# Kernel tuning notes

Measured on AMD Instinct MI355X. Metric: run time of the kernel, lower is better.

## Reference

```python
import jax, jax.numpy as jnp
import numpy as np

N_ELEM = 4
NODES = [384, 1024, 1024, 1]
ALPHA0 = 100.0


def setup_inputs() -> dict:
    key = jax.random.key(0)
    ks = jax.random.split(key, 12)
    B_ref, B_tr, A, D = 32, 64, 128, NODES[0]
    x_ref = jax.random.normal(ks[0], (B_ref, A, D), jnp.float32)
    x_train = jax.random.normal(ks[1], (B_tr, A, D), jnp.float32)
    y_ref = jax.random.normal(ks[2], (B_ref * A,), jnp.float32)
    l_ref = jax.random.randint(ks[3], (B_ref, A), 1, N_ELEM + 1).astype(jnp.int32)
    l_train = jax.random.randint(ks[4], (B_tr, A), 1, N_ELEM + 1).astype(jnp.int32)

    def lin_w(k, fi, fo):
        lim = 1.0 / np.sqrt(fi)
        return jax.random.uniform(k, (N_ELEM, fi, fo), jnp.float32, -lim, lim)

    W1 = lin_w(ks[5], NODES[0], NODES[1])
    b1 = jnp.zeros((N_ELEM, NODES[1]), jnp.float32)
    W2 = lin_w(ks[6], NODES[1], NODES[2])
    b2 = jnp.zeros((N_ELEM, NODES[2]), jnp.float32)
    W3 = lin_w(ks[7], NODES[2], NODES[3])
    b3 = jnp.zeros((N_ELEM, NODES[3]), jnp.float32)
    alpha = jnp.full((N_ELEM,), ALPHA0, jnp.float32)  # one learned alpha per subnet
    return dict(x_ref=x_ref, y_ref=y_ref, l_ref=l_ref, x_train=x_train,
                l_train=l_train, W1=W1, b1=b1, W2=W2, b2=b2, W3=W3, b3=b3,
                alpha=alpha)


def reference(x_ref, y_ref, l_ref, x_train, l_train, W1, b1, W2, b2, W3, b3, alpha):
    D = x_train.shape[-1]
    xr = x_ref.reshape(-1, D)      # [Nref, D]
    xt = x_train.reshape(-1, D)    # [Ntr, D]
    lr = l_ref.reshape(-1)
    lt = l_train.reshape(-1)
    y = jnp.zeros((lt.shape[0],), x_train.dtype)
    for e in range(N_ELEM):        # fixed small loop over element subnets
        label = e + 1

        def mlp(x):
            h = jax.nn.celu(x @ W1[e] + b1[e])
            h = jax.nn.celu(h @ W2[e] + b2[e])
            return h @ W3[e] + b3[e]   # [*, nodes[-1]]

        hr = mlp(xr)               # [Nref, 1]
        ht = mlp(xt)               # [Ntr, 1]
        # pairwise Euclidean distance in the learned 1-d embedding
        d = jnp.sqrt(jnp.sum((ht[:, None, :] - hr[None, :, :]) ** 2, axis=-1))  # [Ntr, Nref]
        # exp kernel restricted to reference atoms of this element
        p = jnp.exp(-alpha[e] * d) * (lr == label).astype(d.dtype)[None, :]
        w = p / jnp.sum(p, axis=1, keepdims=True)
        out_e = w @ y_ref          # [Ntr]
        y = y + jnp.where(lt == label, out_e, 0.0)
    return (l_train, y[:, None])
```

## Files before the change

kernel.cpp:

```cpp
#include <hip/hip_runtime.h>
#include <hip/hip_bf16.h>

#define NREF  4096
#define NTR   8192
#define NCOMB 12288
#define DIN   384
#define HID   1024
#define NE    4
#define ESTR  3456
#define MT    (ESTR / 128)

typedef __attribute__((ext_vector_type(8))) short bf16x8;
typedef __attribute__((ext_vector_type(4))) short s16x4;
typedef __attribute__((ext_vector_type(4))) float f32x4;

#define WS_CNT    0
#define WS_RCNT   16
#define WS_POST   256
#define WS_RIDX   (WS_POST + NTR*4)
#define WS_COMB   (WS_RIDX + NE*NREF*4)
#define WS_W1TH   524288
#define WS_W1TL   (WS_W1TH + NE*DIN*HID*2)
#define WS_XGH    (WS_W1TL + NE*DIN*HID*2)
#define WS_XGL    (WS_XGH + NE*ESTR*DIN*2)
#define WS_W2TH   WS_XGH
#define WS_W2TL   WS_XGL
#define WS_H1H    (WS_XGL + NE*ESTR*DIN*2)
#define WS_H1L    (WS_H1H + (size_t)NE*ESTR*HID*2)
#define WS_HFIN   (WS_H1L + (size_t)NE*ESTR*HID*2)

__device__ __forceinline__ short f2bf(float f) {
    unsigned u = __builtin_bit_cast(unsigned, f);
    unsigned r = (u + 0x7FFF + ((u >> 16) & 1)) >> 16;
    return (short)r;
}
__device__ __forceinline__ float bf2f(short s) {
    unsigned u = ((unsigned)(unsigned short)s) << 16;
    return __builtin_bit_cast(float, u);
}
__device__ __forceinline__ void gload16(const void* g, void* l) {
    __builtin_amdgcn_global_load_lds(
        (const __attribute__((address_space(1))) void*)g,
        (__attribute__((address_space(3))) void*)l, 16, 0, 0);
}
__device__ __forceinline__ float celu1(float v) {
    return v > 0.f ? v : (expf(v) - 1.f);
}

__global__ __launch_bounds__(1024) void k_compact(
    const int* __restrict__ lr, const int* __restrict__ lt,
    int* cnt, int* rcnt, int* comb, int* ridxP, int* post) {
    int t = threadIdx.x;
    int wid = t >> 6, lane = t & 63;
    int base = t * 12;

    int lab[12];
    int c0 = 0, c1 = 0, c2 = 0, c3 = 0;
    int r0 = 0, r1 = 0, r2 = 0, r3 = 0;
#pragma unroll
    for (int j = 0; j < 12; j++) {
        int i = base + j;
        int l = (i < NREF) ? lr[i] : lt[i - NREF];
        lab[j] = l;
        c0 += (l == 1); c1 += (l == 2); c2 += (l == 3); c3 += (l == 4);
        if (i < NREF) {
            r0 += (l == 1); r1 += (l == 2); r2 += (l == 3); r3 += (l == 4);
        }
    }

    int v0 = c0, v1 = c1, v2 = c2, v3 = c3;
#pragma unroll
    for (int off = 1; off < 64; off <<= 1) {
        int u0 = __shfl_up(v0, off, 64), u1 = __shfl_up(v1, off, 64);
        int u2 = __shfl_up(v2, off, 64), u3 = __shfl_up(v3, off, 64);
        if (lane >= off) { v0 += u0; v1 += u1; v2 += u2; v3 += u3; }
    }
    int s0 = r0, s1 = r1, s2 = r2, s3 = r3;
#pragma unroll
    for (int off = 32; off > 0; off >>= 1) {
        s0 += __shfl_xor(s0, off, 64); s1 += __shfl_xor(s1, off, 64);
        s2 += __shfl_xor(s2, off, 64); s3 += __shfl_xor(s3, off, 64);
    }

    __shared__ int wtot[16][4], woff[16][4], rtot[16][4];
    if (lane == 63) {
        wtot[wid][0] = v0; wtot[wid][1] = v1; wtot[wid][2] = v2; wtot[wid][3] = v3;
    }
    if (lane == 0) {
        rtot[wid][0] = s0; rtot[wid][1] = s1; rtot[wid][2] = s2; rtot[wid][3] = s3;
    }
    __syncthreads();
    if (t == 0) {
        int a0 = 0, a1 = 0, a2 = 0, a3 = 0, b0 = 0, b1 = 0, b2 = 0, b3 = 0;
#pragma unroll
        for (int w = 0; w < 16; w++) {
            woff[w][0] = a0; woff[w][1] = a1; woff[w][2] = a2; woff[w][3] = a3;
            a0 += wtot[w][0]; a1 += wtot[w][1]; a2 += wtot[w][2]; a3 += wtot[w][3];
            b0 += rtot[w][0]; b1 += rtot[w][1]; b2 += rtot[w][2]; b3 += rtot[w][3];
        }
        cnt[0] = a0; cnt[1] = a1; cnt[2] = a2; cnt[3] = a3;
        rcnt[0] = b0; rcnt[1] = b1; rcnt[2] = b2; rcnt[3] = b3;
    }
    __syncthreads();

    int q0 = v0 - c0 + woff[wid][0];
    int q1 = v1 - c1 + woff[wid][1];
    int q2 = v2 - c2 + woff[wid][2];
    int q3 = v3 - c3 + woff[wid][3];

#pragma unroll
    for (int j = 0; j < 12; j++) {
        int i = base + j;
        int l = lab[j];
        int p = (l == 1) ? q0 : (l == 2) ? q1 : (l == 3) ? q2 : q3;
        q0 += (l == 1); q1 += (l == 2); q2 += (l == 3); q3 += (l == 4);
        int e = l - 1;
        comb[e * NCOMB + p] = i;
        if (i < NREF) ridxP[e * NREF + p] = i | (p << 16);
        else          post[i - NREF] = p;
    }
}

#define PREP_TR1  1536
#define PREP_GAT  (PREP_TR1 + ESTR/4*NE)
#define PREP_ZERO (PREP_GAT + 4)
__global__ __launch_bounds__(256) void k_prep(
    const float* __restrict__ W1,
    const float* __restrict__ xr, const float* __restrict__ xt,
    const int* __restrict__ cnt, const int* __restrict__ comb,
    short* __restrict__ W1Th, short* __restrict__ W1Tl,
    short* __restrict__ XgH, short* __restrict__ XgL,
    float* __restrict__ hfinC) {
    __shared__ float s[32][33];
    int b = blockIdx.x;
    if (b < PREP_TR1) {
        int e = b / 384, r = b % 384;
        int n0 = (r & 31) * 32, k0 = (r >> 5) * 32;
        int tx = threadIdx.x & 31, ty = threadIdx.x >> 5;
        const float* src = W1 + (size_t)e * DIN * HID;
#pragma unroll
        for (int i = 0; i < 32; i += 8)
            s[ty + i][tx] = src[(size_t)(k0 + ty + i) * HID + n0 + tx];
        __syncthreads();
#pragma unroll
        for (int i = 0; i < 32; i += 8) {
            float v = s[tx][ty + i];
            short hb = f2bf(v);
            short lb = f2bf(v - bf2f(hb));
            size_t o = ((size_t)e * HID + n0 + ty + i) * DIN + k0 + tx;
            W1Th[o] = hb;
            W1Tl[o] = lb;
        }
    } else if (b < PREP_GAT) {
        int b2 = b - PREP_TR1;
        int e = b2 / (ESTR / 4);
        int m = (b2 % (ESTR / 4)) * 4 + (threadIdx.x >> 6);
        int lane = threadIdx.x & 63;
        size_t dst = ((size_t)e * ESTR + m) * DIN;
        if (m < cnt[e]) {
            int g = comb[e * NCOMB + m];
            const float* src = (g < NREF) ? (xr + (size_t)g * DIN)
                                          : (xt + (size_t)(g - NREF) * DIN);
#pragma unroll
            for (int c = lane * 2, it = 0; it < 3; c += 128, ++it) {
                float2 v = *(const float2*)(src + c);
                short2 h, l;
                h.x = f2bf(v.x); l.x = f2bf(v.x - bf2f(h.x));
                h.y = f2bf(v.y); l.y = f2bf(v.y - bf2f(h.y));
                *(short2*)(XgH + dst + c) = h;
                *(short2*)(XgL + dst + c) = l;
            }
        } else {
#pragma unroll
            for (int c = lane * 2, it = 0; it < 3; c += 128, ++it) {
                *(short2*)(XgH + dst + c) = short2{0, 0};
                *(short2*)(XgL + dst + c) = short2{0, 0};
            }
        }
    } else {
        int idx = (b - PREP_GAT) * 1024 + threadIdx.x;
        if (idx * 4 < NE * ESTR) {
            f32x4 z = {0.f, 0.f, 0.f, 0.f};
            *(f32x4*)(hfinC + idx * 4) = z;
        }
    }
}

__global__ __launch_bounds__(256) void k_tr2(const float* __restrict__ W,
                                             short* __restrict__ Th,
                                             short* __restrict__ Tl) {
    int e = blockIdx.z;
    __shared__ float s[32][33];
    int tx = threadIdx.x & 31, ty = threadIdx.x >> 5;
    int k0 = blockIdx.y * 32, n0 = blockIdx.x * 32;
    const float* src = W + (size_t)e * HID * HID;
#pragma unroll
    for (int i = 0; i < 32; i += 8)
        s[ty + i][tx] = src[(size_t)(k0 + ty + i) * HID + n0 + tx];
    __syncthreads();
    int k = k0 + tx;
    int kk = (k & ~63) | ((k & 15) << 2) | ((k >> 4) & 3);
#pragma unroll
    for (int i = 0; i < 32; i += 8) {
        float v = s[tx][ty + i];
        short hb = f2bf(v);
        short lb = f2bf(v - bf2f(hb));
        size_t o = ((size_t)e * HID + n0 + ty + i) * HID + kk;
        Th[o] = hb;
        Tl[o] = lb;
    }
}

#define READ_FRAGS(slotp)                                                     \
    bf16x8 ah[4], al[4], bh[4], bl[4];                                        \
    _Pragma("unroll")                                                         \
    for (int m = 0; m < 4; m++) {                                             \
        int row = wr * 64 + m * 16 + (lane & 15);                             \
        int off = row * 64 + ((((lane >> 4) ^ ((row >> 1) & 3))) << 4);       \
        ah[m] = *(const bf16x8*)((slotp) + off);                              \
        al[m] = *(const bf16x8*)((slotp) + 8192 + off);                       \
    }                                                                         \
    _Pragma("unroll")                                                         \
    for (int n = 0; n < 4; n++) {                                             \
        int row = wc * 64 + n * 16 + (lane & 15);                             \
        int off = row * 64 + ((((lane >> 4) ^ ((row >> 1) & 3))) << 4);       \
        bh[n] = *(const bf16x8*)((slotp) + 16384 + off);                      \
        bl[n] = *(const bf16x8*)((slotp) + 24576 + off);                      \
    }

#define DO_MFMA()                                                             \
    __builtin_amdgcn_s_setprio(1);                                            \
    _Pragma("unroll")                                                         \
    for (int m = 0; m < 4; m++)                                               \
        _Pragma("unroll")                                                     \
        for (int n = 0; n < 4; n++) {                                         \
            acc[m][n] = __builtin_amdgcn_mfma_f32_16x16x32_bf16(ah[m], bh[n], acc[m][n], 0, 0, 0); \
            acc[m][n] = __builtin_amdgcn_mfma_f32_16x16x32_bf16(al[m], bh[n], acc[m][n], 0, 0, 0); \
            acc[m][n] = __builtin_amdgcn_mfma_f32_16x16x32_bf16(ah[m], bl[n], acc[m][n], 0, 0, 0); \
        }                                                                     \
    __builtin_amdgcn_s_setprio(0);

#define PIPE_LOOP(NT, STAGE)                                                  \
    STAGE(0, 0);                                                              \
    for (int kt = 0; kt < (NT); ++kt) {                                       \
        __builtin_amdgcn_sched_barrier(0);                                    \
        asm volatile("s_waitcnt vmcnt(0)" ::: "memory");                      \
        __builtin_amdgcn_s_barrier();                                         \
        __builtin_amdgcn_sched_barrier(0);                                    \
        if (kt + 1 < (NT)) STAGE(kt + 1, (kt + 1) & 1);                       \
        char* slotp = smem + (kt & 1) * 32768;                                \
        READ_FRAGS(slotp)                                                     \
        DO_MFMA()                                                             \
    }

__global__ __launch_bounds__(256) void k_l1(
    const short* __restrict__ XgH, const short* __restrict__ XgL,
    const short* __restrict__ W1Th, const short* __restrict__ W1Tl,
    const float* __restrict__ b1, const int* __restrict__ cnt,
    short* __restrict__ H1h, short* __restrict__ H1l) {
    int bid = blockIdx.x;
    int n0 = (bid & 7) * 128;
    int rest = bid >> 3;
    int e = rest / MT;
    int count = cnt[e];
    int m0 = (rest % MT) * 128;
    if (m0 >= count) return;

    extern __shared__ __align__(16) char smem[];
    int t = threadIdx.x, w = t >> 6, lane = t & 63;
    int wr = w >> 1, wc = w & 1;

    int srow = t >> 2, sx = t & 3, fB = (srow >> 1) & 3;
    size_t aoff0 = ((size_t)e * ESTR + m0 + srow) * DIN + (sx ^ fB) * 8;
    size_t aoff1 = aoff0 + (size_t)64 * DIN;
    size_t boff0 = ((size_t)e * HID + n0 + srow) * DIN + (sx ^ fB) * 8;
    size_t boff1 = boff0 + (size_t)64 * DIN;
    char* ldsW = smem + w * 1024;

#define STAGE1(T, SL) do { int kk = (T) * 32; char* Ld = ldsW + (SL) * 32768; \
        gload16(XgH  + aoff0 + kk, Ld + 0);     gload16(XgH  + aoff1 + kk, Ld + 4096);  \
        gload16(XgL  + aoff0 + kk, Ld + 8192);  gload16(XgL  + aoff1 + kk, Ld + 12288); \
        gload16(W1Th + boff0 + kk, Ld + 16384); gload16(W1Th + boff1 + kk, Ld + 20480); \
        gload16(W1Tl + boff0 + kk, Ld + 24576); gload16(W1Tl + boff1 + kk, Ld + 28672); } while (0)

    f32x4 acc[4][4] = {};
    PIPE_LOOP(DIN / 32, STAGE1)
#undef STAGE1

    int q = lane & 15;
    float bb[4];
#pragma unroll
    for (int n = 0; n < 4; n++) bb[n] = b1[e * HID + n0 + wc * 64 + n * 16 + q];
#pragma unroll
    for (int m = 0; m < 4; m++) {
        int rbase = m0 + wr * 64 + m * 16 + (lane >> 4) * 4;
#pragma unroll
        for (int r = 0; r < 4; r++) {
            int row = rbase + r;
            if (row < count) {
                s16x4 hv, lv;
#pragma unroll
                for (int n = 0; n < 4; n++) {
                    float v = celu1(acc[m][n][r] + bb[n]);
                    hv[n] = f2bf(v);
                    lv[n] = f2bf(v - bf2f(hv[n]));
                }
                size_t o = ((size_t)e * ESTR + row) * HID + n0 + wc * 64 + q * 4;
                *(s16x4*)(H1h + o) = hv;
                *(s16x4*)(H1l + o) = lv;
            }
        }
    }
}

__global__ __launch_bounds__(256) void k_l23(
    const short* __restrict__ H1h, const short* __restrict__ H1l,
    const short* __restrict__ W2Th, const short* __restrict__ W2Tl,
    const float* __restrict__ b2, const float* __restrict__ W3,
    const int* __restrict__ cnt, float* __restrict__ hfinC,
    int mtBase, int mtN) {
    int bid = blockIdx.x;
    int n0 = (bid & 7) * 128;
    int rest = bid >> 3;
    int e = rest / mtN;
    int count = cnt[e];
    int m0 = (mtBase + rest % mtN) * 128;
    if (m0 >= count) return;

    extern __shared__ __align__(16) char smem[];
    int t = threadIdx.x, w = t >> 6, lane = t & 63;
    int wr = w >> 1, wc = w & 1;

    int srow = t >> 2, sx = t & 3, f0 = (srow >> 1) & 3;
    size_t aoff0 = ((size_t)e * ESTR + m0 + srow) * HID + (sx ^ f0) * 8;
    size_t aoff1 = aoff0 + (size_t)64 * HID;
    size_t boff0 = ((size_t)e * HID + n0 + srow) * HID + (sx ^ f0) * 8;
    size_t boff1 = boff0 + (size_t)64 * HID;
    char* ldsW = smem + w * 1024;

#define STAGE23(T, SL) do { int kk = (T) * 32; char* Ld = ldsW + (SL) * 32768; \
        gload16(H1h  + aoff0 + kk, Ld + 0);     gload16(H1h  + aoff1 + kk, Ld + 4096);  \
        gload16(H1l  + aoff0 + kk, Ld + 8192);  gload16(H1l  + aoff1 + kk, Ld + 12288); \
        gload16(W2Th + boff0 + kk, Ld + 16384); gload16(W2Th + boff1 + kk, Ld + 20480); \
        gload16(W2Tl + boff0 + kk, Ld + 24576); gload16(W2Tl + boff1 + kk, Ld + 28672); } while (0)

    f32x4 acc[4][4] = {};
    PIPE_LOOP(HID / 32, STAGE23)
#undef STAGE23

    float s[4][4] = {};
#pragma unroll
    for (int n = 0; n < 4; n++) {
        int col = n0 + wc * 64 + n * 16 + (lane & 15);
        float bbv = b2[e * HID + col];
        float w3 = W3[e * HID + col];
#pragma unroll
        for (int m = 0; m < 4; m++)
#pragma unroll
            for (int r = 0; r < 4; r++)
                s[m][r] += celu1(acc[m][n][r] + bbv) * w3;
    }
#pragma unroll
    for (int m = 0; m < 4; m++)
#pragma unroll
        for (int r = 0; r < 4; r++) {
#pragma unroll
            for (int off = 8; off > 0; off >>= 1)
                s[m][r] += __shfl_xor(s[m][r], off, 64);
        }
    if ((lane & 15) == 0) {
#pragma unroll
        for (int m = 0; m < 4; m++) {
            int rbase = m0 + wr * 64 + m * 16 + (lane >> 4) * 4;
#pragma unroll
            for (int r = 0; r < 4; r++)
                if (rbase + r < count)
                    atomicAdd(&hfinC[e * ESTR + rbase + r], s[m][r]);
        }
    }
}

__global__ __launch_bounds__(256) void k_out(
    const int* __restrict__ lt, const float* __restrict__ yref,
    const float* __restrict__ alpha, const int* __restrict__ rcnt,
    const int* __restrict__ ridxP, const int* __restrict__ post,
    const float* __restrict__ hfinC, float* __restrict__ out) {
    int t = blockIdx.x * 4 + (threadIdx.x >> 6);
    int lane = threadIdx.x & 63;
    if (t >= NTR) return;
    int lab = lt[t];
    int e = lab - 1;
    float ht = hfinC[e * ESTR + post[t]];
    float a = alpha[e];
    int n = rcnt[e];
    const int* lst = ridxP + e * NREF;
    float num = 0.f, den = 0.f;
    for (int i = lane; i < n; i += 64) {
        int pk = lst[i];
        int r = pk & 0xFFFF;
        int pq = pk >> 16;
        float d = fabsf(ht - hfinC[e * ESTR + pq]);
        float p = expf(-a * d);
        num += p * yref[r];
        den += p;
    }
#pragma unroll
    for (int o = 32; o > 0; o >>= 1) {
        num += __shfl_down(num, o, 64);
        den += __shfl_down(den, o, 64);
    }
    if (lane == 0) {
        out[t] = (float)lab;
        out[NTR + t] = num / den;
    }
}

extern "C" void kernel_launch(void* const* d_in, const int* in_sizes, int n_in,
                              void* d_out, int out_size, void* d_ws, size_t ws_size,
                              hipStream_t stream) {
    const float* xr    = (const float*)d_in[0];
    const float* yref  = (const float*)d_in[1];
    const int*   lr    = (const int*)  d_in[2];
    const float* xt    = (const float*)d_in[3];
    const int*   lt    = (const int*)  d_in[4];
    const float* W1    = (const float*)d_in[5];
    const float* b1    = (const float*)d_in[6];
    const float* W2    = (const float*)d_in[7];
    const float* b2    = (const float*)d_in[8];
    const float* W3    = (const float*)d_in[9];
    const float* alpha = (const float*)d_in[11];

    hipFuncSetAttribute((const void*)k_l1,
                        hipFuncAttributeMaxDynamicSharedMemorySize, 2 * 32768);
    hipFuncSetAttribute((const void*)k_l23,
                        hipFuncAttributeMaxDynamicSharedMemorySize, 2 * 32768);

    char* ws = (char*)d_ws;
    int*   cnt   = (int*)(ws + WS_CNT);
    int*   rcnt  = (int*)(ws + WS_RCNT);
    int*   post  = (int*)(ws + WS_POST);
    int*   ridxP = (int*)(ws + WS_RIDX);
    int*   comb  = (int*)(ws + WS_COMB);
    short* W1Th  = (short*)(ws + WS_W1TH);
    short* W1Tl  = (short*)(ws + WS_W1TL);
    short* XgH   = (short*)(ws + WS_XGH);
    short* XgL   = (short*)(ws + WS_XGL);
    short* W2Th  = (short*)(ws + WS_W2TH);
    short* W2Tl  = (short*)(ws + WS_W2TL);
    short* H1h   = (short*)(ws + WS_H1H);
    short* H1l   = (short*)(ws + WS_H1L);
    float* hfinC = (float*)(ws + WS_HFIN);
    float* out   = (float*)d_out;

    k_compact<<<1, 1024, 0, stream>>>(lr, lt, cnt, rcnt, comb, ridxP, post);

    k_prep<<<PREP_ZERO, 256, 0, stream>>>(W1, xr, xt, cnt, comb,
                                          W1Th, W1Tl, XgH, XgL, hfinC);

    k_l1<<<8 * MT * NE, 256, 2 * 32768, stream>>>(XgH, XgL, W1Th, W1Tl, b1, cnt,
                                                  H1h, H1l);

    k_tr2<<<dim3(HID / 32, HID / 32, NE), 256, 0, stream>>>(W2, W2Th, W2Tl);

    k_l23<<<8 * 14 * NE, 256, 2 * 32768, stream>>>(H1h, H1l, W2Th, W2Tl, b2, W3,
                                                   cnt, hfinC, 0, 14);
    k_l23<<<8 * 13 * NE, 256, 2 * 32768, stream>>>(H1h, H1l, W2Th, W2Tl, b2, W3,
                                                   cnt, hfinC, 14, 13);

    k_out<<<NTR / 4, 256, 0, stream>>>(lt, yref, alpha, rcnt, ridxP, post, hfinC, out);
}
```

Baseline: 292.3 us.

## Fuse W2 transpose into prep kernel and compact reference data for output pass

When workspace is large enough, the W2 transpose and bf16 split move into the prep kernel so the XgH/XgL buffers are no longer aliased. This removes the separate k_tr2 launch and the dependency that kept it after k_l1. The two split k_l23 launches are merged into one. k_out now reads compacted hfin and y_ref arrays laid out per element, replacing the packed index list and its gather loads. This costs extra workspace, and the W2 transposed layout here applies a k-swizzle that must match what k_l23 expects.

```diff
diff --git a/kernel.cpp b/kernel.cpp
--- a/kernel.cpp
+++ b/kernel.cpp
@@ -14,21 +14,6 @@
 typedef __attribute__((ext_vector_type(4))) short s16x4;
 typedef __attribute__((ext_vector_type(4))) float f32x4;
 
-#define WS_CNT    0
-#define WS_RCNT   16
-#define WS_POST   256
-#define WS_RIDX   (WS_POST + NTR*4)
-#define WS_COMB   (WS_RIDX + NE*NREF*4)
-#define WS_W1TH   524288
-#define WS_W1TL   (WS_W1TH + NE*DIN*HID*2)
-#define WS_XGH    (WS_W1TL + NE*DIN*HID*2)
-#define WS_XGL    (WS_XGH + NE*ESTR*DIN*2)
-#define WS_W2TH   WS_XGH
-#define WS_W2TL   WS_XGL
-#define WS_H1H    (WS_XGL + NE*ESTR*DIN*2)
-#define WS_H1L    (WS_H1H + (size_t)NE*ESTR*HID*2)
-#define WS_HFIN   (WS_H1L + (size_t)NE*ESTR*HID*2)
-
 __device__ __forceinline__ short f2bf(float f) {
     unsigned u = __builtin_bit_cast(unsigned, f);
     unsigned r = (u + 0x7FFF + ((u >> 16) & 1)) >> 16;
@@ -49,7 +34,7 @@
 
 __global__ __launch_bounds__(1024) void k_compact(
     const int* __restrict__ lr, const int* __restrict__ lt,
-    int* cnt, int* rcnt, int* comb, int* ridxP, int* post) {
+    int* cnt, int* rcnt, int* comb, int* post) {
     int t = threadIdx.x;
     int wid = t >> 6, lane = t & 63;
     int base = t * 12;
@@ -114,26 +99,23 @@
         int l = lab[j];
         int p = (l == 1) ? q0 : (l == 2) ? q1 : (l == 3) ? q2 : q3;
         q0 += (l == 1); q1 += (l == 2); q2 += (l == 3); q3 += (l == 4);
-        int e = l - 1;
-        comb[e * NCOMB + p] = i;
-        if (i < NREF) ridxP[e * NREF + p] = i | (p << 16);
-        else          post[i - NREF] = p;
-    }
-}
-
-#define PREP_TR1  1536
-#define PREP_GAT  (PREP_TR1 + ESTR/4*NE)
-#define PREP_ZERO (PREP_GAT + 4)
+        comb[(l - 1) * NCOMB + p] = i;
+        if (i >= NREF) post[i - NREF] = p;
+    }
+}
+
 __global__ __launch_bounds__(256) void k_prep(
-    const float* __restrict__ W1,
+    const float* __restrict__ W1, const float* __restrict__ W2,
     const float* __restrict__ xr, const float* __restrict__ xt,
+    const float* __restrict__ yref,
     const int* __restrict__ cnt, const int* __restrict__ comb,
     short* __restrict__ W1Th, short* __restrict__ W1Tl,
+    short* __restrict__ W2Th, short* __restrict__ W2Tl,
     short* __restrict__ XgH, short* __restrict__ XgL,
-    float* __restrict__ hfinC) {
+    float* __restrict__ yrefC, float* __restrict__ hfinC, int tr2N) {
     __shared__ float s[32][33];
     int b = blockIdx.x;
-    if (b < PREP_TR1) {
+    if (b < 1536) {
         int e = b / 384, r = b % 384;
         int n0 = (r & 31) * 32, k0 = (r >> 5) * 32;
         int tx = threadIdx.x & 31, ty = threadIdx.x >> 5;
@@ -151,8 +133,29 @@
             W1Th[o] = hb;
             W1Tl[o] = lb;
         }
-    } else if (b < PREP_GAT) {
-        int b2 = b - PREP_TR1;
+    } else if (b < 1536 + tr2N) {
+        int b2 = b - 1536;
+        int e = b2 / 1024, r = b2 % 1024;
+        int n0 = (r & 31) * 32, k0 = (r >> 5) * 32;
+        int tx = threadIdx.x & 31, ty = threadIdx.x >> 5;
+        const float* src = W2 + (size_t)e * HID * HID;
+#pragma unroll
+        for (int i = 0; i < 32; i += 8)
+            s[ty + i][tx] = src[(size_t)(k0 + ty + i) * HID + n0 + tx];
+        __syncthreads();
+        int k = k0 + tx;
+        int kk = (k & ~63) | ((k & 15) << 2) | ((k >> 4) & 3);
+#pragma unroll
+        for (int i = 0; i < 32; i += 8) {
+            float v = s[tx][ty + i];
+            short hb = f2bf(v);
+            short lb = f2bf(v - bf2f(hb));
+            size_t o = ((size_t)e * HID + n0 + ty + i) * HID + kk;
+            W2Th[o] = hb;
+            W2Tl[o] = lb;
+        }
+    } else if (b < 1536 + tr2N + 3456) {
+        int b2 = b - 1536 - tr2N;
         int e = b2 / (ESTR / 4);
         int m = (b2 % (ESTR / 4)) * 4 + (threadIdx.x >> 6);
         int lane = threadIdx.x & 63;
@@ -161,6 +164,7 @@
             int g = comb[e * NCOMB + m];
             const float* src = (g < NREF) ? (xr + (size_t)g * DIN)
                                           : (xt + (size_t)(g - NREF) * DIN);
+            if (lane == 0 && g < NREF) yrefC[e * ESTR + m] = yref[g];
 #pragma unroll
             for (int c = lane * 2, it = 0; it < 3; c += 128, ++it) {
                 float2 v = *(const float2*)(src + c);
@@ -178,7 +182,7 @@
             }
         }
     } else {
-        int idx = (b - PREP_GAT) * 1024 + threadIdx.x;
+        int idx = (b - 1536 - tr2N - 3456) * 1024 + threadIdx.x;
         if (idx * 4 < NE * ESTR) {
             f32x4 z = {0.f, 0.f, 0.f, 0.f};
             *(f32x4*)(hfinC + idx * 4) = z;
@@ -317,14 +321,13 @@
     const short* __restrict__ H1h, const short* __restrict__ H1l,
     const short* __restrict__ W2Th, const short* __restrict__ W2Tl,
     const float* __restrict__ b2, const float* __restrict__ W3,
-    const int* __restrict__ cnt, float* __restrict__ hfinC,
-    int mtBase, int mtN) {
+    const int* __restrict__ cnt, float* __restrict__ hfinC) {
     int bid = blockIdx.x;
     int n0 = (bid & 7) * 128;
     int rest = bid >> 3;
-    int e = rest / mtN;
+    int e = rest / MT;
     int count = cnt[e];
-    int m0 = (mtBase + rest % mtN) * 128;
+    int m0 = (rest % MT) * 128;
     if (m0 >= count) return;
 
     extern __shared__ __align__(16) char smem[];
@@ -381,10 +384,10 @@
 }
 
 __global__ __launch_bounds__(256) void k_out(
-    const int* __restrict__ lt, const float* __restrict__ yref,
-    const float* __restrict__ alpha, const int* __restrict__ rcnt,
-    const int* __restrict__ ridxP, const int* __restrict__ post,
-    const float* __restrict__ hfinC, float* __restrict__ out) {
+    const int* __restrict__ lt, const float* __restrict__ alpha,
+    const int* __restrict__ rcnt, const int* __restrict__ post,
+    const float* __restrict__ hfinC, const float* __restrict__ yrefC,
+    float* __restrict__ out) {
     int t = blockIdx.x * 4 + (threadIdx.x >> 6);
     int lane = threadIdx.x & 63;
     if (t >= NTR) return;
@@ -393,15 +396,13 @@
     float ht = hfinC[e * ESTR + post[t]];
     float a = alpha[e];
     int n = rcnt[e];
-    const int* lst = ridxP + e * NREF;
+    const float* hb = hfinC + e * ESTR;
+    const float* yb = yrefC + e * ESTR;
     float num = 0.f, den = 0.f;
     for (int i = lane; i < n; i += 64) {
-        int pk = lst[i];
-        int r = pk & 0xFFFF;
-        int pq = pk >> 16;
-        float d = fabsf(ht - hfinC[e * ESTR + pq]);
+        float d = fabsf(ht - hb[i]);
         float p = expf(-a * d);
-        num += p * yref[r];
+        num += p * yb[i];
         den += p;
     }
 #pragma unroll
@@ -435,37 +436,55 @@
     hipFuncSetAttribute((const void*)k_l23,
                         hipFuncAttributeMaxDynamicSharedMemorySize, 2 * 32768);
 
+    const size_t SZ_W1T = (size_t)NE * DIN * HID * 2;
+    const size_t SZ_XG  = (size_t)NE * ESTR * DIN * 2;
+    const size_t SZ_W2T = (size_t)NE * HID * HID * 2;
+    const size_t SZ_H1  = (size_t)NE * ESTR * HID * 2;
+
     char* ws = (char*)d_ws;
-    int*   cnt   = (int*)(ws + WS_CNT);
-    int*   rcnt  = (int*)(ws + WS_RCNT);
-    int*   post  = (int*)(ws + WS_POST);
-    int*   ridxP = (int*)(ws + WS_RIDX);
-    int*   comb  = (int*)(ws + WS_COMB);
-    short* W1Th  = (short*)(ws + WS_W1TH);
-    short* W1Tl  = (short*)(ws + WS_W1TL);
-    short* XgH   = (short*)(ws + WS_XGH);
-    short* XgL   = (short*)(ws + WS_XGL);
-    short* W2Th  = (short*)(ws + WS_W2TH);
-    short* W2Tl  = (short*)(ws + WS_W2TL);
-    short* H1h   = (short*)(ws + WS_H1H);
-    short* H1l   = (short*)(ws + WS_H1L);
-    float* hfinC = (float*)(ws + WS_HFIN);
+    int*   cnt   = (int*)(ws + 0);
+    int*   rcnt  = (int*)(ws + 16);
+    int*   post  = (int*)(ws + 256);
+    int*   comb  = (int*)(ws + 256 + (size_t)NTR * 4);
+    size_t off = 262144;
+    short* W1Th = (short*)(ws + off); off += SZ_W1T;
+    short* W1Tl = (short*)(ws + off); off += SZ_W1T;
+    short* XgH  = (short*)(ws + off); off += SZ_XG;
+    short* XgL  = (short*)(ws + off); off += SZ_XG;
+
+    size_t fusedNeed = off + 2 * SZ_W2T + 2 * SZ_H1 + 2 * (size_t)NE * ESTR * 4;
+    bool fused = ws_size >= fusedNeed;
+
+    short *W2Th, *W2Tl;
+    if (fused) {
+        W2Th = (short*)(ws + off); off += SZ_W2T;
+        W2Tl = (short*)(ws + off); off += SZ_W2T;
+    } else {
+        W2Th = XgH;
+        W2Tl = XgL;
+    }
+    short* H1h  = (short*)(ws + off); off += SZ_H1;
+    short* H1l  = (short*)(ws + off); off += SZ_H1;
+    float* hfinC = (float*)(ws + off); off += (size_t)NE * ESTR * 4;
+    float* yrefC = (float*)(ws + off);
     float* out   = (float*)d_out;
 
-    k_compact<<<1, 1024, 0, stream>>>(lr, lt, cnt, rcnt, comb, ridxP, post);
-
-    k_prep<<<PREP_ZERO, 256, 0, stream>>>(W1, xr, xt, cnt, comb,
-                                          W1Th, W1Tl, XgH, XgL, hfinC);
+    int tr2N = fused ? 4096 : 0;
+
+    k_compact<<<1, 1024, 0, stream>>>(lr, lt, cnt, rcnt, comb, post);
+
+    k_prep<<<1536 + tr2N + 3456 + 4, 256, 0, stream>>>(
+        W1, W2, xr, xt, yref, cnt, comb,
+        W1Th, W1Tl, W2Th, W2Tl, XgH, XgL, yrefC, hfinC, tr2N);
 
     k_l1<<<8 * MT * NE, 256, 2 * 32768, stream>>>(XgH, XgL, W1Th, W1Tl, b1, cnt,
                                                   H1h, H1l);
 
-    k_tr2<<<dim3(HID / 32, HID / 32, NE), 256, 0, stream>>>(W2, W2Th, W2Tl);
-
-    k_l23<<<8 * 14 * NE, 256, 2 * 32768, stream>>>(H1h, H1l, W2Th, W2Tl, b2, W3,
-                                                   cnt, hfinC, 0, 14);
-    k_l23<<<8 * 13 * NE, 256, 2 * 32768, stream>>>(H1h, H1l, W2Th, W2Tl, b2, W3,
-                                                   cnt, hfinC, 14, 13);
-
-    k_out<<<NTR / 4, 256, 0, stream>>>(lt, yref, alpha, rcnt, ridxP, post, hfinC, out);
-}
+    if (!fused)
+        k_tr2<<<dim3(HID / 32, HID / 32, NE), 256, 0, stream>>>(W2, W2Th, W2Tl);
+
+    k_l23<<<8 * MT * NE, 256, 2 * 32768, stream>>>(H1h, H1l, W2Th, W2Tl, b2, W3,
+                                                   cnt, hfinC);
+
+    k_out<<<NTR / 4, 256, 0, stream>>>(lt, alpha, rcnt, post, hfinC, yrefC, out);
+}
```

Measured after the change: 276.3 us. 1.06x faster.
